# Performance work log

Measured on AMD Instinct MI355X. Metric: run time of the kernel, lower is better.

Reference implementation:

```python
import jax, jax.numpy as jnp
import numpy as np

D_MODEL = 1024
N_HEADS = 16
D_K = D_MODEL // N_HEADS


def setup_inputs() -> dict:
    key = jax.random.key(0)
    ks = jax.random.split(key, 9)
    s = 0.02
    return {
        "x": jax.random.normal(ks[0], (4, 2048, D_MODEL), dtype=jnp.float32),
        "WQ_w": jax.random.normal(ks[1], (D_MODEL, D_MODEL), dtype=jnp.float32) * s,
        "WQ_b": jax.random.normal(ks[2], (D_MODEL,), dtype=jnp.float32) * s,
        "WK_w": jax.random.normal(ks[3], (D_MODEL, D_MODEL), dtype=jnp.float32) * s,
        "WK_b": jax.random.normal(ks[4], (D_MODEL,), dtype=jnp.float32) * s,
        "WV_w": jax.random.normal(ks[5], (D_MODEL, D_MODEL), dtype=jnp.float32) * s,
        "WV_b": jax.random.normal(ks[6], (D_MODEL,), dtype=jnp.float32) * s,
        "Wo_w": jax.random.normal(ks[7], (D_MODEL, D_MODEL), dtype=jnp.float32) * s,
        "Wo_b": jax.random.normal(ks[8], (D_MODEL,), dtype=jnp.float32) * s,
    }


def _rope_cache(T, dtype):
    half = D_K // 2
    freq = 1.0 / (10000.0 ** (2.0 * jnp.arange(half, dtype=dtype) / D_K))
    angles = jnp.arange(T, dtype=dtype)[:, None] * freq[None, :]  # [T, half]
    return jnp.cos(angles), jnp.sin(angles)


def _apply_rope(x, cos, sin):
    # x: [B, H, T, d_k]; cos/sin: [T, d_k//2] broadcast over B,H
    half = x.shape[-1] // 2
    x1, x2 = x[..., :half], x[..., half:]
    return jnp.concatenate([x1 * cos - x2 * sin, x1 * sin + x2 * cos], axis=-1)


def reference(x, WQ_w, WQ_b, WK_w, WK_b, WV_w, WV_b, Wo_w, Wo_b):
    B, T, D = x.shape

    def proj(w, b):
        y = jnp.einsum('btd,ed->bte', x, w) + b
        return y.reshape(B, T, N_HEADS, D_K).transpose(0, 2, 1, 3)  # [B,H,T,d_k]

    q = proj(WQ_w, WQ_b)
    k = proj(WK_w, WK_b)
    v = proj(WV_w, WV_b)

    cos, sin = _rope_cache(T, x.dtype)
    q = _apply_rope(q, cos, sin)
    k = _apply_rope(k, cos, sin)

    scores = jnp.einsum('bhqd,bhkd->bhqk', q, k) / jnp.sqrt(jnp.asarray(D_K, x.dtype))
    causal = jnp.tril(jnp.ones((T, T), dtype=bool))
    scores = jnp.where(causal[None, None, :, :], scores, -jnp.inf)
    attn = jax.nn.softmax(scores, axis=-1)
    out = jnp.einsum('bhqk,bhkd->bhqd', attn, v)
    out = out.transpose(0, 2, 1, 3).reshape(B, T, D)
    return jnp.einsum('btd,ed->bte', out, Wo_w) + Wo_b
```

## Files before the change

kernel.cpp:

```cpp
#include <hip/hip_runtime.h>
#include <math.h>

#define DM 1024
#define NH 16
#define DK 64
#define BB 4
#define TT 2048
#define MTOT (BB*TT)

typedef __bf16 bf16x8 __attribute__((ext_vector_type(8)));
typedef short  s16x4  __attribute__((ext_vector_type(4)));
typedef short  s16x8  __attribute__((ext_vector_type(8)));
typedef float  f32x4  __attribute__((ext_vector_type(4)));

__device__ __forceinline__ short f2bf_s(float f) {
    __bf16 h = (__bf16)f;
    return __builtin_bit_cast(short, h);
}

__device__ __forceinline__ float exp2_fast(float x) {
    float r;
    asm("v_exp_f32 %0, %1" : "=v"(r) : "v"(x));
    return r;
}

__device__ __forceinline__ void async_copy16(unsigned short* lds, const unsigned short* g) {
    __builtin_amdgcn_global_load_lds(
        (const __attribute__((address_space(1))) unsigned int*)g,
        (__attribute__((address_space(3))) unsigned int*)lds, 16, 0, 0);
}

__global__ __launch_bounds__(256)
void cvt_all_kernel(const float* __restrict__ x,
                    const float* __restrict__ wq, const float* __restrict__ wk,
                    const float* __restrict__ wv, const float* __restrict__ wo,
                    unsigned short* __restrict__ xb,
                    unsigned short* __restrict__ wqb, unsigned short* __restrict__ wkb,
                    unsigned short* __restrict__ wvb, unsigned short* __restrict__ wob)
{
    const int XB = (MTOT * DM) / 1024;
    int bz = blockIdx.x;
    const float* src; unsigned short* dst; int blk;
    if (bz < XB) { src = x; dst = xb; blk = bz; }
    else {
        int t = bz - XB, which = t >> 10;
        blk = t & 1023;
        if (which == 0)      { src = wq; dst = wqb; }
        else if (which == 1) { src = wk; dst = wkb; }
        else if (which == 2) { src = wv; dst = wvb; }
        else                 { src = wo; dst = wob; }
    }
    int i = blk * 256 + threadIdx.x;
    float4 v = ((const float4*)src)[i];
    ushort4 o;
    o.x = (unsigned short)f2bf_s(v.x); o.y = (unsigned short)f2bf_s(v.y);
    o.z = (unsigned short)f2bf_s(v.z); o.w = (unsigned short)f2bf_s(v.w);
    ((ushort4*)dst)[i] = o;
}

template<int MODE>
__global__ __launch_bounds__(256, 3)
void gemm_bf16_kernel(const unsigned short* __restrict__ X,
                      const unsigned short* __restrict__ W0, const float* __restrict__ b0,
                      const unsigned short* __restrict__ W1, const float* __restrict__ b1,
                      const unsigned short* __restrict__ W2, const float* __restrict__ b2,
                      void* __restrict__ Y0, void* __restrict__ Y1, void* __restrict__ Y2)
{
    const unsigned short* W; const float* bias; void* Yv;
    const int z = blockIdx.z;
    if (z == 0)      { W = W0; bias = b0; Yv = Y0; }
    else if (z == 1) { W = W1; bias = b1; Yv = Y1; }
    else             { W = W2; bias = b2; Yv = Y2; }

    __shared__ __align__(16) unsigned short As[128 * 64];
    __shared__ __align__(16) unsigned short Bs[128 * 64];

    const int tid  = threadIdx.x;
    const int w    = tid >> 6, lane = tid & 63;
    const int quad = lane >> 4, lq = lane & 15;
    const int bm = blockIdx.x * 128, bn = blockIdx.y * 128;
    const int wm = (w >> 1) * 64,   wn = (w & 1) * 64;

    const int srow = lane >> 3;
    const int sg   = (lane & 7) ^ srow;
    const int soff = sg * 8;

    f32x4 acc[4][4];
    #pragma unroll
    for (int i = 0; i < 4; ++i)
        #pragma unroll
        for (int j = 0; j < 4; ++j)
            acc[i][j] = {0.f, 0.f, 0.f, 0.f};

    for (int k0 = 0; k0 < DM; k0 += 64) {
        #pragma unroll
        for (int c = 0; c < 4; ++c) {
            int r0 = w * 32 + c * 8;
            async_copy16(&As[r0 * 64], &X[(size_t)(bm + r0 + srow) * DM + k0 + soff]);
            async_copy16(&Bs[r0 * 64], &W[(size_t)(bn + r0 + srow) * DM + k0 + soff]);
        }
        __syncthreads();

        #pragma unroll
        for (int ks = 0; ks < 2; ++ks) {
            const int gsw = ((ks << 2) + quad) ^ (lq & 7);
            bf16x8 af[4], bfr[4];
            #pragma unroll
            for (int i = 0; i < 4; ++i)
                af[i] = *(const bf16x8*)&As[(wm + i*16 + lq) * 64 + gsw * 8];
            #pragma unroll
            for (int j = 0; j < 4; ++j)
                bfr[j] = *(const bf16x8*)&Bs[(wn + j*16 + lq) * 64 + gsw * 8];
            #pragma unroll
            for (int i = 0; i < 4; ++i)
                #pragma unroll
                for (int j = 0; j < 4; ++j)
                    acc[i][j] = __builtin_amdgcn_mfma_f32_16x16x32_bf16(af[i], bfr[j], acc[i][j], 0, 0, 0);
        }
        __syncthreads();
    }

    if (MODE == 0) {
        #pragma unroll
        for (int j = 0; j < 4; ++j) {
            int n = bn + wn + j*16 + lq;
            float bv = bias[n];
            #pragma unroll
            for (int i = 0; i < 4; ++i)
                #pragma unroll
                for (int r = 0; r < 4; ++r) {
                    int m = bm + wm + i*16 + quad*4 + r;
                    ((float*)Yv)[(size_t)m * DM + n] = acc[i][j][r] + bv;
                }
        }
    } else if (z == 2) {
        #pragma unroll
        for (int j = 0; j < 4; ++j) {
            int n = bn + wn + j*16 + lq;
            float bv = bias[n];
            int h = n >> 6, dk = n & 63;
            #pragma unroll
            for (int i = 0; i < 4; ++i) {
                int m0 = bm + wm + i*16 + quad*4;
                int b = m0 >> 11, t0 = m0 & 2047;
                int u0 = t0 & 63;
                int t0n = (t0 & ~63) | (((u0 >> 5) & 1) << 5)
                        | (((u0 >> 2) & 3) << 3) | (((u0 >> 4) & 1) << 2);
                ushort4 o;
                o.x = (unsigned short)f2bf_s(acc[i][j][0] + bv);
                o.y = (unsigned short)f2bf_s(acc[i][j][1] + bv);
                o.z = (unsigned short)f2bf_s(acc[i][j][2] + bv);
                o.w = (unsigned short)f2bf_s(acc[i][j][3] + bv);
                *(ushort4*)&((unsigned short*)Yv)[((size_t)(b * NH + h) * DK + dk) * TT + t0n] = o;
            }
        }
    } else {
        const float QSC = (z == 0) ? 0.125f * 1.44269504f : 1.0f;
        const int h = (bn + wn) >> 6;
        const int b = (bm + wm) >> 11;
        const int tb0 = ((bm + wm) & 2047) + quad * 4;
        #pragma unroll
        for (int jp = 0; jp < 2; ++jp) {
            int dk1 = jp * 16 + lq;
            float freq = exp2f(-(float)dk1 * 0.4152410118f);
            float bv1 = bias[bn + wn + dk1];
            float bv2 = bias[bn + wn + dk1 + 32];
            float s1, c1, s16v, c16v, sb, cb;
            __sincosf(freq, &s1, &c1);
            __sincosf(16.0f * freq, &s16v, &c16v);
            __sincosf((float)tb0 * freq, &sb, &cb);
            #pragma unroll
            for (int i = 0; i < 4; ++i) {
                float cr = cb, sr = sb;
                #pragma unroll
                for (int r = 0; r < 4; ++r) {
                    int t = tb0 + i*16 + r;
                    float v1 = acc[i][jp][r]     + bv1;
                    float v2 = acc[i][jp + 2][r] + bv2;
                    float o1 = (v1 * cr - v2 * sr) * QSC;
                    float o2 = (v1 * sr + v2 * cr) * QSC;
                    size_t base = ((size_t)(b * NH + h) * TT + t) << 6;
                    unsigned int pk = (unsigned int)(unsigned short)f2bf_s(o1)
                                    | ((unsigned int)(unsigned short)f2bf_s(o2) << 16);
                    *(unsigned int*)&((unsigned short*)Yv)[base + 2*dk1] = pk;
                    float cn = cr * c1 - sr * s1;
                    sr = cr * s1 + sr * c1;
                    cr = cn;
                }
                float cbn = cb * c16v - sb * s16v;
                sb = cb * s16v + sb * c16v;
                cb = cbn;
            }
        }
    }
}

__global__ __launch_bounds__(256, 4)
void attn_kernel(const unsigned short* __restrict__ Q, const unsigned short* __restrict__ K,
                 const unsigned short* __restrict__ Vt_g, unsigned short* __restrict__ ctx)
{
    __shared__ __align__(16) unsigned short KV[2][2][64 * 64];

    const int tid  = threadIdx.x;
    const int w    = tid >> 6, lane = tid & 63;
    const int quad = lane >> 4, lq = lane & 15;
    const int bh = blockIdx.x;
    const int qt = 31 - blockIdx.y;
    const size_t kbase = (size_t)bh * TT * DK;
    const size_t vbase = (size_t)bh * DK * TT;

    const int srow = lane >> 3;
    const int sg   = (lane & 7) ^ srow;
    const unsigned short* Ksrc = &K[kbase + (size_t)(w*16 + srow) * DK + sg*8];
    const unsigned short* Vsrc = &Vt_g[vbase + (size_t)(w*16 + srow) * TT + sg*8];

    auto issue = [&](int kb, int buf) {
        unsigned short* Kd = &KV[buf][0][w*16*64];
        unsigned short* Vd = &KV[buf][1][w*16*64];
        const unsigned short* ks0 = Ksrc + (size_t)kb * 64 * DK;
        const unsigned short* vs0 = Vsrc + (size_t)kb * 64;
        async_copy16(Kd,          ks0);
        async_copy16(Kd + 8*64,   ks0 + 8*DK);
        async_copy16(Vd,          vs0);
        async_copy16(Vd + 8*64,   vs0 + (size_t)8*TT);
    };

    const int qrow = qt*64 + w*16 + lq;
    bf16x8 qf[2];
    qf[0] = *(const bf16x8*)&Q[kbase + (size_t)qrow * DK + quad*8];
    qf[1] = *(const bf16x8*)&Q[kbase + (size_t)qrow * DK + 32 + quad*8];

    const s16x4 ones = {(short)0x3F80, (short)0x3F80, (short)0x3F80, (short)0x3F80};
    f32x4 accO[4];
    f32x4 accL = {0.f, 0.f, 0.f, 0.f};
    #pragma unroll
    for (int dt = 0; dt < 4; ++dt) accO[dt] = {0.f,0.f,0.f,0.f};

    issue(0, 0);
    for (int kb = 0; kb <= qt; ++kb) {
        __syncthreads();
        if (kb < qt) issue(kb + 1, (kb + 1) & 1);

        const unsigned short* Kb_ = &KV[kb & 1][0][0];
        const unsigned short* Vb_ = &KV[kb & 1][1][0];

        f32x4 st[4];
        #pragma unroll
        for (int nt = 0; nt < 4; ++nt) st[nt] = {0.f,0.f,0.f,0.f};
        #pragma unroll
        for (int ks = 0; ks < 2; ++ks) {
            bf16x8 kfh[4];
            #pragma unroll
            for (int nt = 0; nt < 4; ++nt)
                kfh[nt] = *(const bf16x8*)&Kb_[(nt*16 + lq) * 64 +
                                (((ks << 2) + quad) ^ (lq & 7)) * 8];
            __builtin_amdgcn_s_setprio(1);
            #pragma unroll
            for (int nt = 0; nt < 4; ++nt)
                st[nt] = __builtin_amdgcn_mfma_f32_16x16x32_bf16(kfh[nt], qf[ks], st[nt], 0, 0, 0);
            __builtin_amdgcn_s_setprio(0);
        }
        if (kb == qt) {
            #pragma unroll
            for (int nt = 0; nt < 4; ++nt)
                #pragma unroll
                for (int r = 0; r < 4; ++r) {
                    int kc = kb*64 + nt*16 + quad*4 + r;
                    if (kc > qrow) st[nt][r] = -1e30f;
                }
        }
        s16x4 p[4];
        #pragma unroll
        for (int nt = 0; nt < 4; ++nt)
            #pragma unroll
            for (int r = 0; r < 4; ++r)
                p[nt][r] = f2bf_s(exp2_fast(st[nt][r]));

        #pragma unroll
        for (int P = 0; P < 2; ++P) {
            s16x8 vf[4];
            #pragma unroll
            for (int dt = 0; dt < 4; ++dt)
                vf[dt] = *(const s16x8*)&Vb_[(dt*16 + lq) * 64 +
                                (((P << 2) + quad) ^ (lq & 7)) * 8];
            __builtin_amdgcn_s_setprio(1);
            #pragma unroll
            for (int k2 = 0; k2 < 2; ++k2) {
                const int kt = P*2 + k2;
                accL = __builtin_amdgcn_mfma_f32_16x16x16bf16_1k(p[kt], ones, accL, 0, 0, 0);
                #pragma unroll
                for (int dt = 0; dt < 4; ++dt) {
                    s16x4 vs;
                    if (k2) vs = __builtin_shufflevector(vf[dt], vf[dt], 4, 5, 6, 7);
                    else    vs = __builtin_shufflevector(vf[dt], vf[dt], 0, 1, 2, 3);
                    accO[dt] = __builtin_amdgcn_mfma_f32_16x16x16bf16_1k(
                        p[kt], vs, accO[dt], 0, 0, 0);
                }
            }
            __builtin_amdgcn_s_setprio(0);
        }
    }

    const int b = bh >> 4, h = bh & 15;
    f32x4 il4;
    #pragma unroll
    for (int r = 0; r < 4; ++r) il4[r] = 1.0f / accL[r];
    #pragma unroll
    for (int r = 0; r < 4; ++r) {
        int t = qt*64 + w*16 + quad*4 + r;
        size_t ob = ((size_t)b * TT + t) * DM + h * DK;
        #pragma unroll
        for (int dt = 0; dt < 4; ++dt)
            ((__bf16*)ctx)[ob + dt*16 + lq] = (__bf16)(accO[dt][r] * il4[r]);
    }
}

extern "C" void kernel_launch(void* const* d_in, const int* in_sizes, int n_in,
                              void* d_out, int out_size, void* d_ws, size_t ws_size,
                              hipStream_t stream)
{
    const float* x   = (const float*)d_in[0];
    const float* WQw = (const float*)d_in[1];
    const float* WQb = (const float*)d_in[2];
    const float* WKw = (const float*)d_in[3];
    const float* WKb = (const float*)d_in[4];
    const float* WVw = (const float*)d_in[5];
    const float* WVb = (const float*)d_in[6];
    const float* WOw = (const float*)d_in[7];
    const float* WOb = (const float*)d_in[8];
    float* out = (float*)d_out;

    unsigned short* ws  = (unsigned short*)d_ws;
    unsigned short* xb  = ws;
    unsigned short* wqb = xb  + (size_t)MTOT * DM;
    unsigned short* wkb = wqb + (size_t)DM * DM;
    unsigned short* wvb = wkb + (size_t)DM * DM;
    unsigned short* wob = wvb + (size_t)DM * DM;
    unsigned short* Qb  = wob + (size_t)DM * DM;
    unsigned short* Kb  = Qb  + (size_t)MTOT * DM;
    unsigned short* Vb  = Kb  + (size_t)MTOT * DM;
    unsigned short* Vtb = Vb  + (size_t)MTOT * DM;
    unsigned short* ctxb = Vb;

    cvt_all_kernel<<<(MTOT*DM)/1024 + 4*(DM*DM)/1024, 256, 0, stream>>>(
        x, WQw, WKw, WVw, WOw, xb, wqb, wkb, wvb, wob);

    gemm_bf16_kernel<1><<<dim3(MTOT/128, DM/128, 3), 256, 0, stream>>>(
        xb, wqb, WQb, wkb, WKb, wvb, WVb, Qb, Kb, Vtb);

    attn_kernel<<<dim3(BB*NH, 32), 256, 0, stream>>>(Qb, Kb, Vtb, ctxb);

    gemm_bf16_kernel<0><<<dim3(MTOT/128, DM/128, 1), 256, 0, stream>>>(
        ctxb, wob, WOb, wob, WOb, wob, WOb, out, out, out);
}
```

Baseline: 226.9 us.

## Double-buffer GEMM shared-memory tiles with K=32 stages to overlap loads

Splits the GEMM K loop into 32-wide stages with two shared-memory buffers, so the async copy of the next stage is issued before the MFMAs on the current one. This aims to hide global-load latency behind compute and removes one of the two barriers per iteration. Shared memory per block stays the same, but there are twice as many iterations and barriers, each doing half the MFMA work. The swizzle pattern is redesigned for the 32-wide rows.

```diff
diff --git a/kernel.cpp b/kernel.cpp
--- a/kernel.cpp
+++ b/kernel.cpp
@@ -72,8 +72,8 @@
     else if (z == 1) { W = W1; bias = b1; Yv = Y1; }
     else             { W = W2; bias = b2; Yv = Y2; }
 
-    __shared__ __align__(16) unsigned short As[128 * 64];
-    __shared__ __align__(16) unsigned short Bs[128 * 64];
+    __shared__ __align__(16) unsigned short As[2][128 * 32];
+    __shared__ __align__(16) unsigned short Bs[2][128 * 32];
 
     const int tid  = threadIdx.x;
     const int w    = tid >> 6, lane = tid & 63;
@@ -81,9 +81,20 @@
     const int bm = blockIdx.x * 128, bn = blockIdx.y * 128;
     const int wm = (w >> 1) * 64,   wn = (w & 1) * 64;
 
-    const int srow = lane >> 3;
-    const int sg   = (lane & 7) ^ srow;
-    const int soff = sg * 8;
+    const int srowS = lane >> 2;
+    const int sgS   = (lane & 3) ^ ((lane >> 3) & 3);
+
+    auto stage = [&](int t, int buf) {
+        const int k0 = t * 32;
+        #pragma unroll
+        for (int c = 0; c < 2; ++c) {
+            int r0 = c * 64 + w * 16;
+            async_copy16(&As[buf][r0 * 32],
+                         &X[(size_t)(bm + r0 + srowS) * DM + k0 + sgS * 8]);
+            async_copy16(&Bs[buf][r0 * 32],
+                         &W[(size_t)(bn + r0 + srowS) * DM + k0 + sgS * 8]);
+        }
+    };
 
     f32x4 acc[4][4];
     #pragma unroll
@@ -92,32 +103,27 @@
         for (int j = 0; j < 4; ++j)
             acc[i][j] = {0.f, 0.f, 0.f, 0.f};
 
-    for (int k0 = 0; k0 < DM; k0 += 64) {
-        #pragma unroll
-        for (int c = 0; c < 4; ++c) {
-            int r0 = w * 32 + c * 8;
-            async_copy16(&As[r0 * 64], &X[(size_t)(bm + r0 + srow) * DM + k0 + soff]);
-            async_copy16(&Bs[r0 * 64], &W[(size_t)(bn + r0 + srow) * DM + k0 + soff]);
-        }
+    const int gsw = quad ^ ((lq >> 1) & 3);
+
+    stage(0, 0);
+    for (int t = 0; t < DM / 32; ++t) {
         __syncthreads();
-
-        #pragma unroll
-        for (int ks = 0; ks < 2; ++ks) {
-            const int gsw = ((ks << 2) + quad) ^ (lq & 7);
-            bf16x8 af[4], bfr[4];
-            #pragma unroll
-            for (int i = 0; i < 4; ++i)
-                af[i] = *(const bf16x8*)&As[(wm + i*16 + lq) * 64 + gsw * 8];
+        if (t + 1 < DM / 32) stage(t + 1, (t + 1) & 1);
+
+        const unsigned short* Ab = &As[t & 1][0];
+        const unsigned short* Bb = &Bs[t & 1][0];
+        bf16x8 af[4], bfr[4];
+        #pragma unroll
+        for (int i = 0; i < 4; ++i)
+            af[i] = *(const bf16x8*)&Ab[(wm + i*16 + lq) * 32 + gsw * 8];
+        #pragma unroll
+        for (int j = 0; j < 4; ++j)
+            bfr[j] = *(const bf16x8*)&Bb[(wn + j*16 + lq) * 32 + gsw * 8];
+        #pragma unroll
+        for (int i = 0; i < 4; ++i)
             #pragma unroll
             for (int j = 0; j < 4; ++j)
-                bfr[j] = *(const bf16x8*)&Bs[(wn + j*16 + lq) * 64 + gsw * 8];
-            #pragma unroll
-            for (int i = 0; i < 4; ++i)
-                #pragma unroll
-                for (int j = 0; j < 4; ++j)
-                    acc[i][j] = __builtin_amdgcn_mfma_f32_16x16x32_bf16(af[i], bfr[j], acc[i][j], 0, 0, 0);
-        }
-        __syncthreads();
+                acc[i][j] = __builtin_amdgcn_mfma_f32_16x16x32_bf16(af[i], bfr[j], acc[i][j], 0, 0, 0);
     }
 
     if (MODE == 0) {
```

After: 244.0 us. 7.6% more time.
